# Optimization experiments

Hardware: AMD Instinct MI355X
Metric: run time of the kernel (lower is better)

## Reference

```python
import jax, jax.numpy as jnp
import numpy as np

B, N, H, DH, E, D_IN = 2, 2048, 8, 32, 65536, 256
O = H * DH
SCALE = float(np.sqrt(DH))


def setup_inputs() -> dict:
    key = jax.random.key(0)
    ks = jax.random.split(key, 8)
    rng = np.random.default_rng(0)
    x = jax.random.normal(ks[0], (B, N, D_IN), jnp.float32)
    adj = jax.random.uniform(ks[1], (B, N, N), jnp.float32)
    # unique edges per graph so scatter-add matches torch advanced-index +=
    flat = np.stack([rng.choice(N * N, size=E, replace=False) for _ in range(B)])
    edge_index = jnp.asarray(np.stack([flat // N, flat % N], axis=1), jnp.int32)  # [B,2,E]
    edge_attr = jax.random.normal(ks[2], (B, E, H), jnp.float32)
    mask = jnp.ones((B, N), dtype=bool)
    qkv_w = jax.random.normal(ks[3], (D_IN, 3 * O), jnp.float32) / np.sqrt(D_IN)
    qkv_b = jnp.zeros((3 * O,), jnp.float32)
    e_w1 = jax.random.normal(ks[4], (H, H), jnp.float32) / np.sqrt(H)
    e_b1 = jnp.zeros((H,), jnp.float32)
    e_w2 = jax.random.normal(ks[5], (H, H), jnp.float32) / np.sqrt(H)
    e_b2 = jnp.zeros((H,), jnp.float32)
    shifts = jnp.asarray(np.linspace(0.1, 0.8, H), jnp.float32).reshape(1, H, 1, 1)
    widths = jnp.full((1, H, 1, 1), 0.5, jnp.float32)
    self_loop_W = jnp.asarray(1.0 / DH + rng.uniform(0, 1, H), jnp.float32).reshape(1, H, 1, 1)
    return dict(x=x, adj=adj, edge_attr=edge_attr, qkv_w=qkv_w, qkv_b=qkv_b,
                e_w1=e_w1, e_b1=e_b1, e_w2=e_w2, e_b2=e_b2,
                shifts=shifts, widths=widths, self_loop_W=self_loop_W,
                edge_index=edge_index, mask=mask)


def reference(x, adj, edge_attr, qkv_w, qkv_b, e_w1, e_b1, e_w2, e_b2,
              shifts, widths, self_loop_W, edge_index, mask):
    Bq, Nq = x.shape[0], x.shape[1]
    # qkv projection -> [3,B,H,N,DH]
    qkv = (x @ qkv_w + qkv_b).reshape(Bq, Nq, 3, H, DH)
    qkv = jnp.transpose(qkv, (2, 0, 3, 1, 4))
    Q, K, V = qkv[0], qkv[1], qkv[2]
    # edge FFN applied twice (eval mode: noise/dropout are identity)
    def ffn(e):
        return jax.nn.relu(e @ e_w1 + e_b1) @ e_w2 + e_b2
    ea = ffn(ffn(edge_attr))                      # [B,E,H]
    ea = jnp.transpose(ea, (0, 2, 1))             # [B,H,E]
    # scores + learned moire adjacency bias
    scores = jnp.einsum('bhqd,bhkd->bhqk', Q, K) / SCALE
    moire = jnp.exp(-((adj[:, None] - shifts) ** 2) / (2.0 * widths ** 2))  # gaussian focus
    moire = jnp.clip(moire, 1e-6, None)
    s = scores + jnp.log(moire)                   # [B,H,N,N]
    # scatter edge features into score matrix
    u = edge_index[:, 0, :]                        # [B,E]
    v = edge_index[:, 1, :]
    bi = jnp.arange(Bq)[:, None, None]
    hi = jnp.arange(H)[None, :, None]
    s = s.at[bi, hi, u[:, None, :], v[:, None, :]].add(ea)
    # self-loop diagonal bias (non-trainable)
    s = s + jnp.eye(Nq, dtype=s.dtype)[None, None] * self_loop_W
    # mask and softmax
    m2 = mask[:, None, :] & mask[:, :, None]       # [B,N,N]
    s = jnp.where(m2[:, None], s, jnp.asarray(-1e6, s.dtype))
    attn = jax.nn.softmax(s, axis=-1)
    out = jnp.einsum('bhqk,bhkd->bhqd', attn, V)
    return jnp.transpose(out, (0, 2, 1, 3)).reshape(Bq, Nq, O)
```

## Files before the change

kernel.cpp:

```cpp
#include <hip/hip_runtime.h>

#define B_ 2
#define N_ 2048
#define H_ 8
#define DH_ 32
#define E_ 65536
#define DIN_ 256
#define KT 256
#define NKT (N_ / KT)
#define ECAP 32
#define QSCALE 0.2550348872f
#define LOG2E 1.4426950408889634f
#define LOG2MIN -19.931568569324174f

typedef short bf16x8 __attribute__((ext_vector_type(8)));
typedef float floatx4 __attribute__((ext_vector_type(4)));

__device__ __forceinline__ unsigned short f2b(float f){
  union { float f; unsigned int u; } v; v.f = f;
  return (unsigned short)((v.u + 0x7fffu + ((v.u >> 16) & 1u)) >> 16);
}
__device__ __forceinline__ bf16x8 f8_to_bf(const float* p){
  float4 a = *(const float4*)p, b = *(const float4*)(p + 4);
  bf16x8 r;
// ... 25 lines not shown
    __shared__ float W1[64], W2[64], Bv1[8], Bv2[8];
    if (tid < 64){ W1[tid] = w1[tid]; W2[tid] = w2[tid]; }
    if (tid < 8){ Bv1[tid] = b1[tid]; Bv2[tid] = b2[tid]; }
    __syncthreads();
    int gid = bb * 256 + tid;
    const float* ep = eattr + (size_t)gid * 8;
    float cur[8];
#pragma unroll
    for (int i = 0; i < 8; ++i) cur[i] = ep[i];
#pragma unroll
    for (int pass = 0; pass < 2; ++pass){
      float t[8];
#pragma unroll
      for (int j = 0; j < 8; ++j){
        float s = Bv1[j];
#pragma unroll
        for (int i = 0; i < 8; ++i) s += cur[i] * W1[i * 8 + j];
        t[j] = fmaxf(s, 0.f);
      }
#pragma unroll
      for (int j = 0; j < 8; ++j){
        float s = Bv2[j];
#pragma unroll
        for (int i = 0; i < 8; ++i) s += t[i] * W2[i * 8 + j];
        cur[j] = s;
      }
    }
    float* op = ea + (size_t)gid * 8;
#pragma unroll
    for (int j = 0; j < 8; ++j) op[j] = cur[j] * LOG2E;
  } else if (bb < 1024){
    int gid = (bb - 512) * 256 + tid;
    int b = gid >> 16, e = gid & (E_ - 1);
    int u = ei[(size_t)b * 2 * E_ + e];
    int v = ei[(size_t)b * 2 * E_ + E_ + e];
    int bucket = ((b << 11) + u) * 8 + (v >> 8);
    int slot = atomicAdd(&cnt[bucket], 1);
    if (slot < ECAP) pck[(size_t)bucket * ECAP + slot] = ((unsigned int)e << 11) | (unsigned int)v;
  } else {
    int k = bb - 1024;
    for (int c = tid; c < 768; c += 256)
      wT[(size_t)c * 256 + k] = f2b(w[(size_t)k * 768 + c]);
  }
}

__global__ __launch_bounds__(256) void qkv_kernel(
    const float* __restrict__ x, const unsigned short* __restrict__ wT,
    const float* __restrict__ bias,
    unsigned short* __restrict__ Qb, unsigned short* __restrict__ Kb, unsigned short* __restrict__ Vt)
{
  int tid = threadIdx.x;
  int wave = tid >> 6, lane = tid & 63, m = lane & 15, quad = lane >> 4;
  int rowbase = blockIdx.x * 16;
  int colbase = blockIdx.y * 64 + wave * 16;
  floatx4 acc = {0.f, 0.f, 0.f, 0.f};
#pragma unroll
  for (int kb = 0; kb < 8; ++kb){
    bf16x8 af = f8_to_bf(x + (size_t)(rowbase + m) * DIN_ + kb * 32 + quad * 8);
    bf16x8 bf = *(const bf16x8*)(wT + (size_t)(colbase + m) * DIN_ + kb * 32 + quad * 8);
    acc = __builtin_amdgcn_mfma_f32_16x16x32_bf16(af, bf, acc, 0, 0, 0);
  }
  int ccol = colbase + m;
  int which = ccol >> 8, hh = (ccol >> 5) & 7, dh = ccol & 31;
  float bv = bias[ccol];
  int row0 = rowbase + quad * 4;
  int bidx = row0 >> 11, n0 = row0 & (N_ - 1);
  size_t bh = (size_t)(bidx * H_ + hh);
  if (which == 0){
#pragma unroll
    for (int r = 0; r < 4; ++r)
      Qb[(bh * N_ + n0 + r) * DH_ + dh] = f2b((acc[r] + bv) * QSCALE);
  } else if (which == 1){
#pragma unroll
    for (int r = 0; r < 4; ++r)
      Kb[(bh * N_ + n0 + r) * DH_ + dh] = f2b(acc[r] + bv);
  } else {
    ushort4 st;
    st.x = f2b(acc[0] + bv); st.y = f2b(acc[1] + bv);
    st.z = f2b(acc[2] + bv); st.w = f2b(acc[3] + bv);
    *(ushort4*)(Vt + (bh * DH_ + dh) * N_ + n0) = st;
  }
}

__global__ __launch_bounds__(256) void attn_kernel(
    const unsigned short* __restrict__ Qb, const unsigned short* __restrict__ Kb,
    const unsigned short* __restrict__ Vt, const float* __restrict__ adj,
    const float* __restrict__ ea, const int* __restrict__ cnt, const unsigned int* __restrict__ pck,
    const float* __restrict__ shifts, const float* __restrict__ widths,
    const float* __restrict__ selfW, float* __restrict__ out)
{
  __shared__ float S[4][16][68];
  __shared__ float mfin[4][16], lfin[4][16];

  int bid = blockIdx.x;
  int qt = bid & 127, h = (bid >> 7) & 7, b = bid >> 10;
  int qbase = qt * 16;
  int tid = threadIdx.x, wave = tid >> 6, lane = tid & 63, m = lane & 15, quad = lane >> 4;
  float shift_h = shifts[h];
  float w_h = widths[h];
  float i2w_h = LOG2E / (2.f * w_h * w_h);
  float selfW_h = selfW[h] * LOG2E;
  size_t krow = (size_t)(b * H_ + h) * N_;
  size_t vrow = (size_t)(b * H_ + h) * DH_;
  bf16x8 qfrag = *(const bf16x8*)(Qb + (krow + qbase + m) * DH_ + quad * 8);
  float (*Sw)[68] = S[wave];
  int wcol = wave * 64;

  int rr = lane >> 2, sl0 = lane & 3;
  const int* cntp = cnt + ((size_t)(b * N_) + qbase + rr) * 8;
  const unsigned int* pckp = pck + ((size_t)((b * N_ + qbase + rr) * 8)) * ECAP;
  const float* eabase = ea + (size_t)b * E_ * H_ + h;
  const float* adjp = adj + ((size_t)b * N_ + qbase + m) * N_ + wcol + quad * 8;
  const unsigned short* vp0 = Vt + (vrow + m) * N_ + wcol + quad * 8;
  const unsigned short* vp1 = Vt + (vrow + 16 + m) * N_ + wcol + quad * 8;
  const unsigned short* kp  = Kb + (krow + wcol + m) * DH_ + quad * 8;

  floatx4 sh4 = {shift_h, shift_h, shift_h, shift_h};
  floatx4 ni4 = {-i2w_h, -i2w_h, -i2w_h, -i2w_h};
  floatx4 lm4 = {LOG2MIN, LOG2MIN, LOG2MIN, LOG2MIN};

  float mcur = -1e30f, lcur = 0.f;
  floatx4 oacc0 = {0.f, 0.f, 0.f, 0.f};
  floatx4 oacc1 = {0.f, 0.f, 0.f, 0.f};

  int nb_c = cntp[0]; nb_c = nb_c > ECAP ? ECAP : nb_c;
  unsigned int pk0 = pckp[sl0];
  unsigned int pk1 = pckp[sl0 + 4];
  int c0_c = (int)(pk0 & (N_ - 1)) - wcol;
  int c1_c = (int)(pk1 & (N_ - 1)) - wcol;
  bool g0_c = (sl0 < nb_c) && ((unsigned)c0_c < 64u);
  bool g1_c = (sl0 + 4 < nb_c) && ((unsigned)c1_c < 64u);
  float ea0_c = 0.f, ea1_c = 0.f;
  if (g0_c) ea0_c = eabase[(size_t)(pk0 >> 11) * H_];
  if (g1_c) ea1_c = eabase[(size_t)(pk1 >> 11) * H_];

#pragma unroll
  for (int kt = 0; kt < NKT; ++kt){
    int k0 = kt * KT;
    int nb_n = 0; unsigned int pk0_n = 0, pk1_n = 0;
    if (kt + 1 < NKT){
      nb_n  = cntp[kt + 1];
      pk0_n = pckp[(kt + 1) * ECAP + sl0];
      pk1_n = pckp[(kt + 1) * ECAP + sl0 + 4];
    }
    const float* ap = adjp + k0;
    floatx4 a00 = *(const floatx4*)(ap);
    floatx4 a01 = *(const floatx4*)(ap + 4);
    floatx4 a10 = *(const floatx4*)(ap + 32);
    floatx4 a11 = *(const floatx4*)(ap + 36);

#pragma unroll
    for (int s = 0; s < 4; ++s){
      bf16x8 kf = *(const bf16x8*)(kp + (size_t)(k0 + s * 16) * DH_);
      floatx4 acc = {0.f, 0.f, 0.f, 0.f};
      acc = __builtin_amdgcn_mfma_f32_16x16x32_bf16(qfrag, kf, acc, 0, 0, 0);
#pragma unroll
      for (int r = 0; r < 4; ++r)
        Sw[quad * 4 + r][s * 16 + m] = acc[r];
    }
    {
      int dw = qbase - k0 - wcol;
      if ((unsigned)dw < 64u && lane < 16)
        Sw[lane][dw + lane] += selfW_h;
    }
    if (g0_c) Sw[rr][c0_c] += ea0_c;
    if (g1_c) Sw[rr][c1_c] += ea1_c;
    if (nb_c > 8){
      for (int slot = sl0 + 8; slot < nb_c; slot += 4){
        unsigned int p = pckp[kt * ECAP + slot];
        int vv = (int)(p & (N_ - 1));
        int c = vv - k0 - wcol;
        if ((unsigned)c < 64u) Sw[rr][c] += eabase[(size_t)(p >> 11) * H_];
      }
    }
    int c0_n = 0, c1_n = 0; bool g0_n = false, g1_n = false;
    float ea0_n = 0.f, ea1_n = 0.f;
    if (kt + 1 < NKT){
      nb_n = nb_n > ECAP ? ECAP : nb_n;
      c0_n = (int)(pk0_n & (N_ - 1)) - (k0 + KT) - wcol;
      c1_n = (int)(pk1_n & (N_ - 1)) - (k0 + KT) - wcol;
      g0_n = (sl0 < nb_n) && ((unsigned)c0_n < 64u);
      g1_n = (sl0 + 4 < nb_n) && ((unsigned)c1_n < 64u);
      if (g0_n) ea0_n = eabase[(size_t)(pk0_n >> 11) * H_];
      if (g1_n) ea1_n = eabase[(size_t)(pk1_n >> 11) * H_];
    }
    bf16x8 vf00 = *(const bf16x8*)(vp0 + k0);
    bf16x8 vf01 = *(const bf16x8*)(vp1 + k0);
    bf16x8 vf10 = *(const bf16x8*)(vp0 + k0 + 32);
    bf16x8 vf11 = *(const bf16x8*)(vp1 + k0 + 32);

    const float* sp = &Sw[m][quad * 8];
    floatx4 s00 = *(const floatx4*)(sp);
    floatx4 s01 = *(const floatx4*)(sp + 4);
    floatx4 s10 = *(const floatx4*)(sp + 32);
    floatx4 s11 = *(const floatx4*)(sp + 36);
    floatx4 d;
    d = a00 - sh4; s00 += __builtin_elementwise_max(d * d * ni4, lm4);
    d = a01 - sh4; s01 += __builtin_elementwise_max(d * d * ni4, lm4);
    d = a10 - sh4; s10 += __builtin_elementwise_max(d * d * ni4, lm4);
    d = a11 - sh4; s11 += __builtin_elementwise_max(d * d * ni4, lm4);
    float lm = fmaxf(fmaxf(fmaxf(s00.x, s00.y), fmaxf(s00.z, s00.w)),
                     fmaxf(fmaxf(s01.x, s01.y), fmaxf(s01.z, s01.w)));
    lm = fmaxf(lm, fmaxf(fmaxf(fmaxf(s10.x, s10.y), fmaxf(s10.z, s10.w)),
                         fmaxf(fmaxf(s11.x, s11.y), fmaxf(s11.z, s11.w))));
    lm = fmaxf(lm, __shfl_xor(lm, 16));
    lm = fmaxf(lm, __shfl_xor(lm, 32));
    float mnew = fmaxf(mcur, lm);
    float al = fexp2(mcur - mnew);
    mcur = mnew;
    float al0 = __shfl(al, quad * 4 + 0);
    float al1 = __shfl(al, quad * 4 + 1);
    float al2 = __shfl(al, quad * 4 + 2);
    float al3 = __shfl(al, quad * 4 + 3);
    oacc0[0] *= al0; oacc0[1] *= al1; oacc0[2] *= al2; oacc0[3] *= al3;
    oacc1[0] *= al0; oacc1[1] *= al1; oacc1[2] *= al2; oacc1[3] *= al3;
    floatx4 m4 = {mcur, mcur, mcur, mcur};
    floatx4 e0v = s00 - m4, e1v = s01 - m4, e2v = s10 - m4, e3v = s11 - m4;
    float ps = 0.f, p0, p1;
    union { bf16x8 v; unsigned int u[4]; } P;
    p0 = fexp2(e0v.x); p1 = fexp2(e0v.y); ps += p0 + p1; P.u[0] = cvt_pk_bf16(p0, p1);
    p0 = fexp2(e0v.z); p1 = fexp2(e0v.w); ps += p0 + p1; P.u[1] = cvt_pk_bf16(p0, p1);
    p0 = fexp2(e1v.x); p1 = fexp2(e1v.y); ps += p0 + p1; P.u[2] = cvt_pk_bf16(p0, p1);
    p0 = fexp2(e1v.z); p1 = fexp2(e1v.w); ps += p0 + p1; P.u[3] = cvt_pk_bf16(p0, p1);
    oacc0 = __builtin_amdgcn_mfma_f32_16x16x32_bf16(P.v, vf00, oacc0, 0, 0, 0);
    oacc1 = __builtin_amdgcn_mfma_f32_16x16x32_bf16(P.v, vf01, oacc1, 0, 0, 0);
    p0 = fexp2(e2v.x); p1 = fexp2(e2v.y); ps += p0 + p1; P.u[0] = cvt_pk_bf16(p0, p1);
    p0 = fexp2(e2v.z); p1 = fexp2(e2v.w); ps += p0 + p1; P.u[1] = cvt_pk_bf16(p0, p1);
    p0 = fexp2(e3v.x); p1 = fexp2(e3v.y); ps += p0 + p1; P.u[2] = cvt_pk_bf16(p0, p1);
    p0 = fexp2(e3v.z); p1 = fexp2(e3v.w); ps += p0 + p1; P.u[3] = cvt_pk_bf16(p0, p1);
    oacc0 = __builtin_amdgcn_mfma_f32_16x16x32_bf16(P.v, vf10, oacc0, 0, 0, 0);
    oacc1 = __builtin_amdgcn_mfma_f32_16x16x32_bf16(P.v, vf11, oacc1, 0, 0, 0);
    ps += __shfl_xor(ps, 16);
    ps += __shfl_xor(ps, 32);
    lcur = lcur * al + ps;
    nb_c = nb_n; g0_c = g0_n; g1_c = g1_n;
    c0_c = c0_n; c1_c = c1_n; ea0_c = ea0_n; ea1_c = ea1_n;
  }

  if (quad == 0){ mfin[wave][m] = mcur; lfin[wave][m] = lcur; }
  float* Ow = &S[wave][0][0];
#pragma unroll
  for (int r = 0; r < 4; ++r){
    Ow[(quad * 4 + r) * 32 + m]      = oacc0[r];
    Ow[(quad * 4 + r) * 32 + 16 + m] = oacc1[r];
  }
  __syncthreads();
  const float* Sv = &S[0][0][0];
#pragma unroll
  for (int ii = 0; ii < 2; ++ii){
    int i = tid + ii * 256;
    int r = i >> 5, dcol = i & 31;
    float m0 = mfin[0][r], m1 = mfin[1][r], m2 = mfin[2][r], m3 = mfin[3][r];
    float mg = fmaxf(fmaxf(m0, m1), fmaxf(m2, m3));
    float w0 = fexp2(m0 - mg), w1 = fexp2(m1 - mg);
    float w2 = fexp2(m2 - mg), w3 = fexp2(m3 - mg);
    int o_idx = r * 32 + dcol;
    float o = Sv[o_idx] * w0 + Sv[1088 + o_idx] * w1
            + Sv[2176 + o_idx] * w2 + Sv[3264 + o_idx] * w3;
    float l = lfin[0][r] * w0 + lfin[1][r] * w1 + lfin[2][r] * w2 + lfin[3][r] * w3;
    out[((size_t)b * N_ + qbase + r) * (H_ * DH_) + h * DH_ + dcol] = o / l;
  }
}

extern "C" void kernel_launch(void* const* d_in, const int* in_sizes, int n_in,
                              void* d_out, int out_size, void* d_ws, size_t ws_size,
                              hipStream_t stream)
{
  const float* x      = (const float*)d_in[0];
  const float* adj    = (const float*)d_in[1];
  const float* eattr  = (const float*)d_in[2];
  const float* qkvw   = (const float*)d_in[3];
  const float* qkvb   = (const float*)d_in[4];
  const float* ew1    = (const float*)d_in[5];
  const float* eb1    = (const float*)d_in[6];
  const float* ew2    = (const float*)d_in[7];
  const float* eb2    = (const float*)d_in[8];
  const float* shifts = (const float*)d_in[9];
  const float* widths = (const float*)d_in[10];
  const float* selfW  = (const float*)d_in[11];
  const int*   ei     = (const int*)d_in[12];
  float* out = (float*)d_out;

  char* ws = (char*)d_ws;
  unsigned short* Qb  = (unsigned short*)(ws);
  unsigned short* Kb  = (unsigned short*)(ws + ((size_t)2 << 20));
  unsigned short* Vt  = (unsigned short*)(ws + ((size_t)4 << 20));
  unsigned short* wT  = (unsigned short*)(ws + ((size_t)6 << 20));
  float*          ea  = (float*)(ws + ((size_t)7 << 20));
  int*            cnt = (int*)(ws + ((size_t)11 << 20));
  unsigned int*  pck  = (unsigned int*)(ws + ((size_t)12 << 20));

  hipMemsetAsync(cnt, 0, (size_t)B_ * N_ * 8 * sizeof(int), stream);
  hipLaunchKernelGGL(prep_kernel, dim3(1280), dim3(256), 0, stream,
                     eattr, ew1, eb1, ew2, eb2, ea, ei, cnt, pck, qkvw, wT);
  hipLaunchKernelGGL(qkv_kernel, dim3(256, 12), dim3(256), 0, stream, x, wT, qkvb, Qb, Kb, Vt);
  hipLaunchKernelGGL(attn_kernel, dim3(B_ * H_ * (N_ / 16)), dim3(256), 0, stream,
                     Qb, Kb, Vt, adj, ea, cnt, pck, shifts, widths, selfW, out);
}
```

Before: 235.0 us.

## Keep QK scores in registers via transposed MFMA; stage only sparse deltas in LDS

Computes K·Qᵀ with swapped MFMA operands so each lane holds score columns directly in registers in the layout the P·V MFMA needs. This removes the per-tile round trip of the full score tile through shared memory. Sparse edge and self-loop biases now go into a small per-wave delta buffer in LDS, which is read, zeroed and refilled one tile ahead. In exchange, adj and V are loaded as narrower strided ushort4/float4 pieces, and B fragments are assembled by hand in registers.

```diff
diff --git a/kernel.cpp b/kernel.cpp
--- a/kernel.cpp
+++ b/kernel.cpp
@@ -138,7 +138,7 @@
     const float* __restrict__ shifts, const float* __restrict__ widths,
     const float* __restrict__ selfW, float* __restrict__ out)
 {
-  __shared__ float S[4][16][68];
+  __shared__ float Dlt[4][16][68];
   __shared__ float mfin[4][16], lfin[4][16];
 
   int bid = blockIdx.x;
@@ -152,17 +152,40 @@
   size_t krow = (size_t)(b * H_ + h) * N_;
   size_t vrow = (size_t)(b * H_ + h) * DH_;
   bf16x8 qfrag = *(const bf16x8*)(Qb + (krow + qbase + m) * DH_ + quad * 8);
-  float (*Sw)[68] = S[wave];
+  float (*Dw)[68] = Dlt[wave];
   int wcol = wave * 64;
+
+  floatx4 z4 = {0.f, 0.f, 0.f, 0.f};
+  float* dp0 = &Dw[m][quad * 4];
+  *(floatx4*)(dp0)      = z4;
+  *(floatx4*)(dp0 + 16) = z4;
+  *(floatx4*)(dp0 + 32) = z4;
+  *(floatx4*)(dp0 + 48) = z4;
 
   int rr = lane >> 2, sl0 = lane & 3;
   const int* cntp = cnt + ((size_t)(b * N_) + qbase + rr) * 8;
   const unsigned int* pckp = pck + ((size_t)((b * N_ + qbase + rr) * 8)) * ECAP;
   const float* eabase = ea + (size_t)b * E_ * H_ + h;
-  const float* adjp = adj + ((size_t)b * N_ + qbase + m) * N_ + wcol + quad * 8;
-  const unsigned short* vp0 = Vt + (vrow + m) * N_ + wcol + quad * 8;
-  const unsigned short* vp1 = Vt + (vrow + 16 + m) * N_ + wcol + quad * 8;
+  const float* adjp = adj + ((size_t)b * N_ + qbase + m) * N_ + wcol + quad * 4;
+  const unsigned short* vpA = Vt + (vrow + m) * N_ + wcol + quad * 4;
+  const unsigned short* vpB = Vt + (vrow + 16 + m) * N_ + wcol + quad * 4;
   const unsigned short* kp  = Kb + (krow + wcol + m) * DH_ + quad * 8;
+
+  int ktd = qbase >> 8;
+
+  {
+    int nb0 = cntp[0]; nb0 = nb0 > ECAP ? ECAP : nb0;
+    for (int slot = sl0; slot < nb0; slot += 4){
+      unsigned int p = pckp[slot];
+      int c = (int)(p & (N_ - 1)) - wcol;
+      if ((unsigned)c < 64u)
+        Dw[rr][c] += eabase[(size_t)(p >> 11) * H_];
+    }
+    if (ktd == 0 && lane < 16){
+      int cd = qbase + lane - wcol;
+      if ((unsigned)cd < 64u) Dw[lane][cd] += selfW_h;
+    }
+  }
 
   floatx4 sh4 = {shift_h, shift_h, shift_h, shift_h};
   floatx4 ni4 = {-i2w_h, -i2w_h, -i2w_h, -i2w_h};
@@ -172,20 +195,17 @@
   floatx4 oacc0 = {0.f, 0.f, 0.f, 0.f};
   floatx4 oacc1 = {0.f, 0.f, 0.f, 0.f};
 
-  int nb_c = cntp[0]; nb_c = nb_c > ECAP ? ECAP : nb_c;
-  unsigned int pk0 = pckp[sl0];
-  unsigned int pk1 = pckp[sl0 + 4];
-  int c0_c = (int)(pk0 & (N_ - 1)) - wcol;
-  int c1_c = (int)(pk1 & (N_ - 1)) - wcol;
-  bool g0_c = (sl0 < nb_c) && ((unsigned)c0_c < 64u);
-  bool g1_c = (sl0 + 4 < nb_c) && ((unsigned)c1_c < 64u);
-  float ea0_c = 0.f, ea1_c = 0.f;
-  if (g0_c) ea0_c = eabase[(size_t)(pk0 >> 11) * H_];
-  if (g1_c) ea1_c = eabase[(size_t)(pk1 >> 11) * H_];
-
 #pragma unroll
   for (int kt = 0; kt < NKT; ++kt){
     int k0 = kt * KT;
+    floatx4 d0 = *(const floatx4*)(dp0);
+    floatx4 d1 = *(const floatx4*)(dp0 + 16);
+    floatx4 d2 = *(const floatx4*)(dp0 + 32);
+    floatx4 d3 = *(const floatx4*)(dp0 + 48);
+    *(floatx4*)(dp0)      = z4;
+    *(floatx4*)(dp0 + 16) = z4;
+    *(floatx4*)(dp0 + 32) = z4;
+    *(floatx4*)(dp0 + 48) = z4;
     int nb_n = 0; unsigned int pk0_n = 0, pk1_n = 0;
     if (kt + 1 < NKT){
       nb_n  = cntp[kt + 1];
@@ -193,65 +213,43 @@
       pk1_n = pckp[(kt + 1) * ECAP + sl0 + 4];
     }
     const float* ap = adjp + k0;
-    floatx4 a00 = *(const floatx4*)(ap);
-    floatx4 a01 = *(const floatx4*)(ap + 4);
-    floatx4 a10 = *(const floatx4*)(ap + 32);
-    floatx4 a11 = *(const floatx4*)(ap + 36);
-
-#pragma unroll
-    for (int s = 0; s < 4; ++s){
-      bf16x8 kf = *(const bf16x8*)(kp + (size_t)(k0 + s * 16) * DH_);
-      floatx4 acc = {0.f, 0.f, 0.f, 0.f};
-      acc = __builtin_amdgcn_mfma_f32_16x16x32_bf16(qfrag, kf, acc, 0, 0, 0);
-#pragma unroll
-      for (int r = 0; r < 4; ++r)
-        Sw[quad * 4 + r][s * 16 + m] = acc[r];
-    }
-    {
-      int dw = qbase - k0 - wcol;
-      if ((unsigned)dw < 64u && lane < 16)
-        Sw[lane][dw + lane] += selfW_h;
-    }
-    if (g0_c) Sw[rr][c0_c] += ea0_c;
-    if (g1_c) Sw[rr][c1_c] += ea1_c;
-    if (nb_c > 8){
-      for (int slot = sl0 + 8; slot < nb_c; slot += 4){
-        unsigned int p = pckp[kt * ECAP + slot];
-        int vv = (int)(p & (N_ - 1));
-        int c = vv - k0 - wcol;
-        if ((unsigned)c < 64u) Sw[rr][c] += eabase[(size_t)(p >> 11) * H_];
-      }
-    }
+    floatx4 a0 = *(const floatx4*)(ap);
+    floatx4 a1 = *(const floatx4*)(ap + 16);
+    floatx4 a2 = *(const floatx4*)(ap + 32);
+    floatx4 a3 = *(const floatx4*)(ap + 48);
+    bf16x8 kf0 = *(const bf16x8*)(kp + (size_t)(k0)      * DH_);
+    bf16x8 kf1 = *(const bf16x8*)(kp + (size_t)(k0 + 16) * DH_);
+    bf16x8 kf2 = *(const bf16x8*)(kp + (size_t)(k0 + 32) * DH_);
+    bf16x8 kf3 = *(const bf16x8*)(kp + (size_t)(k0 + 48) * DH_);
+    floatx4 s0 = __builtin_amdgcn_mfma_f32_16x16x32_bf16(kf0, qfrag, z4, 0, 0, 0);
+    floatx4 s1 = __builtin_amdgcn_mfma_f32_16x16x32_bf16(kf1, qfrag, z4, 0, 0, 0);
+    floatx4 s2 = __builtin_amdgcn_mfma_f32_16x16x32_bf16(kf2, qfrag, z4, 0, 0, 0);
+    floatx4 s3 = __builtin_amdgcn_mfma_f32_16x16x32_bf16(kf3, qfrag, z4, 0, 0, 0);
+    const unsigned short* vA = vpA + k0;
+    const unsigned short* vB = vpB + k0;
+    ushort4 vA0 = *(const ushort4*)(vA);      ushort4 vA1 = *(const ushort4*)(vA + 16);
+    ushort4 vA2 = *(const ushort4*)(vA + 32); ushort4 vA3 = *(const ushort4*)(vA + 48);
+    ushort4 vB0 = *(const ushort4*)(vB);      ushort4 vB1 = *(const ushort4*)(vB + 16);
+    ushort4 vB2 = *(const ushort4*)(vB + 32); ushort4 vB3 = *(const ushort4*)(vB + 48);
     int c0_n = 0, c1_n = 0; bool g0_n = false, g1_n = false;
     float ea0_n = 0.f, ea1_n = 0.f;
     if (kt + 1 < NKT){
       nb_n = nb_n > ECAP ? ECAP : nb_n;
-      c0_n = (int)(pk0_n & (N_ - 1)) - (k0 + KT) - wcol;
-      c1_n = (int)(pk1_n & (N_ - 1)) - (k0 + KT) - wcol;
-      g0_n = (sl0 < nb_n) && ((unsigned)c0_n < 64u);
-      g1_n = (sl0 + 4 < nb_n) && ((unsigned)c1_n < 64u);
+      c0_n = (int)(pk0_n & (N_ - 1)) - wcol;
+      c1_n = (int)(pk1_n & (N_ - 1)) - wcol;
+      g0_n = (sl0 < nb_n) && ((unsigned)(c0_n - (k0 + KT)) < 64u);
+      g1_n = (sl0 + 4 < nb_n) && ((unsigned)(c1_n - (k0 + KT)) < 64u);
       if (g0_n) ea0_n = eabase[(size_t)(pk0_n >> 11) * H_];
       if (g1_n) ea1_n = eabase[(size_t)(pk1_n >> 11) * H_];
     }
-    bf16x8 vf00 = *(const bf16x8*)(vp0 + k0);
-    bf16x8 vf01 = *(const bf16x8*)(vp1 + k0);
-    bf16x8 vf10 = *(const bf16x8*)(vp0 + k0 + 32);
-    bf16x8 vf11 = *(const bf16x8*)(vp1 + k0 + 32);
-
-    const float* sp = &Sw[m][quad * 8];
-    floatx4 s00 = *(const floatx4*)(sp);
-    floatx4 s01 = *(const floatx4*)(sp + 4);
-    floatx4 s10 = *(const floatx4*)(sp + 32);
-    floatx4 s11 = *(const floatx4*)(sp + 36);
-    floatx4 d;
-    d = a00 - sh4; s00 += __builtin_elementwise_max(d * d * ni4, lm4);
-    d = a01 - sh4; s01 += __builtin_elementwise_max(d * d * ni4, lm4);
-    d = a10 - sh4; s10 += __builtin_elementwise_max(d * d * ni4, lm4);
-    d = a11 - sh4; s11 += __builtin_elementwise_max(d * d * ni4, lm4);
-    float lm = fmaxf(fmaxf(fmaxf(s00.x, s00.y), fmaxf(s00.z, s00.w)),
-                     fmaxf(fmaxf(s01.x, s01.y), fmaxf(s01.z, s01.w)));
-    lm = fmaxf(lm, fmaxf(fmaxf(fmaxf(s10.x, s10.y), fmaxf(s10.z, s10.w)),
-                         fmaxf(fmaxf(s11.x, s11.y), fmaxf(s11.z, s11.w))));
+    floatx4 t;
+    t = a0 - sh4; s0 += d0 + __builtin_elementwise_max(t * t * ni4, lm4);
+    t = a1 - sh4; s1 += d1 + __builtin_elementwise_max(t * t * ni4, lm4);
+    t = a2 - sh4; s2 += d2 + __builtin_elementwise_max(t * t * ni4, lm4);
+    t = a3 - sh4; s3 += d3 + __builtin_elementwise_max(t * t * ni4, lm4);
+    floatx4 mxv = __builtin_elementwise_max(__builtin_elementwise_max(s0, s1),
+                                            __builtin_elementwise_max(s2, s3));
+    float lm = fmaxf(fmaxf(mxv.x, mxv.y), fmaxf(mxv.z, mxv.w));
     lm = fmaxf(lm, __shfl_xor(lm, 16));
     lm = fmaxf(lm, __shfl_xor(lm, 32));
     float mnew = fmaxf(mcur, lm);
@@ -263,38 +261,60 @@
     float al3 = __shfl(al, quad * 4 + 3);
     oacc0[0] *= al0; oacc0[1] *= al1; oacc0[2] *= al2; oacc0[3] *= al3;
     oacc1[0] *= al0; oacc1[1] *= al1; oacc1[2] *= al2; oacc1[3] *= al3;
-    floatx4 m4 = {mcur, mcur, mcur, mcur};
-    floatx4 e0v = s00 - m4, e1v = s01 - m4, e2v = s10 - m4, e3v = s11 - m4;
-    float ps = 0.f, p0, p1;
-    union { bf16x8 v; unsigned int u[4]; } P;
-    p0 = fexp2(e0v.x); p1 = fexp2(e0v.y); ps += p0 + p1; P.u[0] = cvt_pk_bf16(p0, p1);
-    p0 = fexp2(e0v.z); p1 = fexp2(e0v.w); ps += p0 + p1; P.u[1] = cvt_pk_bf16(p0, p1);
-    p0 = fexp2(e1v.x); p1 = fexp2(e1v.y); ps += p0 + p1; P.u[2] = cvt_pk_bf16(p0, p1);
-    p0 = fexp2(e1v.z); p1 = fexp2(e1v.w); ps += p0 + p1; P.u[3] = cvt_pk_bf16(p0, p1);
-    oacc0 = __builtin_amdgcn_mfma_f32_16x16x32_bf16(P.v, vf00, oacc0, 0, 0, 0);
-    oacc1 = __builtin_amdgcn_mfma_f32_16x16x32_bf16(P.v, vf01, oacc1, 0, 0, 0);
-    p0 = fexp2(e2v.x); p1 = fexp2(e2v.y); ps += p0 + p1; P.u[0] = cvt_pk_bf16(p0, p1);
-    p0 = fexp2(e2v.z); p1 = fexp2(e2v.w); ps += p0 + p1; P.u[1] = cvt_pk_bf16(p0, p1);
-    p0 = fexp2(e3v.x); p1 = fexp2(e3v.y); ps += p0 + p1; P.u[2] = cvt_pk_bf16(p0, p1);
-    p0 = fexp2(e3v.z); p1 = fexp2(e3v.w); ps += p0 + p1; P.u[3] = cvt_pk_bf16(p0, p1);
-    oacc0 = __builtin_amdgcn_mfma_f32_16x16x32_bf16(P.v, vf10, oacc0, 0, 0, 0);
-    oacc1 = __builtin_amdgcn_mfma_f32_16x16x32_bf16(P.v, vf11, oacc1, 0, 0, 0);
+    floatx4 mb = {mcur, mcur, mcur, mcur};
+    floatx4 e0 = s0 - mb, e1 = s1 - mb, e2 = s2 - mb, e3 = s3 - mb;
+    floatx4 p0, p1, p2, p3;
+    p0.x = fexp2(e0.x); p0.y = fexp2(e0.y); p0.z = fexp2(e0.z); p0.w = fexp2(e0.w);
+    p1.x = fexp2(e1.x); p1.y = fexp2(e1.y); p1.z = fexp2(e1.z); p1.w = fexp2(e1.w);
+    p2.x = fexp2(e2.x); p2.y = fexp2(e2.y); p2.z = fexp2(e2.z); p2.w = fexp2(e2.w);
+    p3.x = fexp2(e3.x); p3.y = fexp2(e3.y); p3.z = fexp2(e3.z); p3.w = fexp2(e3.w);
+    floatx4 psv = (p0 + p1) + (p2 + p3);
+    float ps = (psv.x + psv.y) + (psv.z + psv.w);
+    union { bf16x8 v; unsigned int u[4]; } A0, A1;
+    A0.u[0] = cvt_pk_bf16(p0.x, p0.y); A0.u[1] = cvt_pk_bf16(p0.z, p0.w);
+    A0.u[2] = cvt_pk_bf16(p1.x, p1.y); A0.u[3] = cvt_pk_bf16(p1.z, p1.w);
+    A1.u[0] = cvt_pk_bf16(p2.x, p2.y); A1.u[1] = cvt_pk_bf16(p2.z, p2.w);
+    A1.u[2] = cvt_pk_bf16(p3.x, p3.y); A1.u[3] = cvt_pk_bf16(p3.z, p3.w);
+    bf16x8 B00, B01, B10, B11;
+    B00[0] = (short)vA0.x; B00[1] = (short)vA0.y; B00[2] = (short)vA0.z; B00[3] = (short)vA0.w;
+    B00[4] = (short)vA1.x; B00[5] = (short)vA1.y; B00[6] = (short)vA1.z; B00[7] = (short)vA1.w;
+    B01[0] = (short)vB0.x; B01[1] = (short)vB0.y; B01[2] = (short)vB0.z; B01[3] = (short)vB0.w;
+    B01[4] = (short)vB1.x; B01[5] = (short)vB1.y; B01[6] = (short)vB1.z; B01[7] = (short)vB1.w;
+    B10[0] = (short)vA2.x; B10[1] = (short)vA2.y; B10[2] = (short)vA2.z; B10[3] = (short)vA2.w;
+    B10[4] = (short)vA3.x; B10[5] = (short)vA3.y; B10[6] = (short)vA3.z; B10[7] = (short)vA3.w;
+    B11[0] = (short)vB2.x; B11[1] = (short)vB2.y; B11[2] = (short)vB2.z; B11[3] = (short)vB2.w;
+    B11[4] = (short)vB3.x; B11[5] = (short)vB3.y; B11[6] = (short)vB3.z; B11[7] = (short)vB3.w;
+    oacc0 = __builtin_amdgcn_mfma_f32_16x16x32_bf16(A0.v, B00, oacc0, 0, 0, 0);
+    oacc1 = __builtin_amdgcn_mfma_f32_16x16x32_bf16(A0.v, B01, oacc1, 0, 0, 0);
+    oacc0 = __builtin_amdgcn_mfma_f32_16x16x32_bf16(A1.v, B10, oacc0, 0, 0, 0);
+    oacc1 = __builtin_amdgcn_mfma_f32_16x16x32_bf16(A1.v, B11, oacc1, 0, 0, 0);
     ps += __shfl_xor(ps, 16);
     ps += __shfl_xor(ps, 32);
     lcur = lcur * al + ps;
-    nb_c = nb_n; g0_c = g0_n; g1_c = g1_n;
-    c0_c = c0_n; c1_c = c1_n; ea0_c = ea0_n; ea1_c = ea1_n;
+    if (g0_n) Dw[rr][c0_n - (k0 + KT)] += ea0_n;
+    if (g1_n) Dw[rr][c1_n - (k0 + KT)] += ea1_n;
+    if (nb_n > 8){
+      for (int slot = sl0 + 8; slot < nb_n; slot += 4){
+        unsigned int p = pckp[(kt + 1) * ECAP + slot];
+        int c = (int)(p & (N_ - 1)) - (k0 + KT) - wcol;
+        if ((unsigned)c < 64u) Dw[rr][c] += eabase[(size_t)(p >> 11) * H_];
+      }
+    }
+    if (kt + 1 == ktd && lane < 16){
+      int cd = qbase + lane - (kt + 1) * KT - wcol;
+      if ((unsigned)cd < 64u) Dw[lane][cd] += selfW_h;
+    }
   }
 
   if (quad == 0){ mfin[wave][m] = mcur; lfin[wave][m] = lcur; }
-  float* Ow = &S[wave][0][0];
+  float* Ow = &Dlt[wave][0][0];
 #pragma unroll
   for (int r = 0; r < 4; ++r){
     Ow[(quad * 4 + r) * 32 + m]      = oacc0[r];
     Ow[(quad * 4 + r) * 32 + 16 + m] = oacc1[r];
   }
   __syncthreads();
-  const float* Sv = &S[0][0][0];
+  const float* Sv = &Dlt[0][0][0];
 #pragma unroll
   for (int ii = 0; ii < 2; ++ii){
     int i = tid + ii * 256;
```

Measured after the change: 260.7 us. 11.0% more time.

## Process two 16-row query tiles per attention block and remap blocks across XCDs

Applied to the files above, without the earlier changes.

Each attention block now handles 32 query rows as two independent 16-row chains that share the K and V fragment loads. This halves the global loads of K and V per query row. Block indices are also remapped so that all heads of the same query region land on the same XCD, which should improve L2 reuse of the adjacency and edge data. In exchange the block uses more registers and twice the shared memory, launches half as many blocks, and adds a launch-bounds occupancy hint.

```diff
diff --git a/kernel.cpp b/kernel.cpp
--- a/kernel.cpp
+++ b/kernel.cpp
@@ -131,19 +131,22 @@
   }
 }
 
-__global__ __launch_bounds__(256) void attn_kernel(
+__global__ __launch_bounds__(256, 4) void attn_kernel(
     const unsigned short* __restrict__ Qb, const unsigned short* __restrict__ Kb,
     const unsigned short* __restrict__ Vt, const float* __restrict__ adj,
     const float* __restrict__ ea, const int* __restrict__ cnt, const unsigned int* __restrict__ pck,
     const float* __restrict__ shifts, const float* __restrict__ widths,
     const float* __restrict__ selfW, float* __restrict__ out)
 {
-  __shared__ float S[4][16][68];
-  __shared__ float mfin[4][16], lfin[4][16];
+  __shared__ float S2[2][4][16][68];
+  __shared__ float mfin[2][4][16], lfin[2][4][16];
 
   int bid = blockIdx.x;
-  int qt = bid & 127, h = (bid >> 7) & 7, b = bid >> 10;
-  int qbase = qt * 16;
+  int xcd = bid & 7, idx = bid >> 3;
+  int h = idx & 7;
+  int bqp = xcd * 16 + (idx >> 3);
+  int b = bqp >> 6, qp = bqp & 63;
+  int qbaseA = qp * 32, qbaseB = qbaseA + 16;
   int tid = threadIdx.x, wave = tid >> 6, lane = tid & 63, m = lane & 15, quad = lane >> 4;
   float shift_h = shifts[h];
   float w_h = widths[h];
@@ -151,15 +154,20 @@
   float selfW_h = selfW[h] * LOG2E;
   size_t krow = (size_t)(b * H_ + h) * N_;
   size_t vrow = (size_t)(b * H_ + h) * DH_;
-  bf16x8 qfrag = *(const bf16x8*)(Qb + (krow + qbase + m) * DH_ + quad * 8);
-  float (*Sw)[68] = S[wave];
+  bf16x8 qfragA = *(const bf16x8*)(Qb + (krow + qbaseA + m) * DH_ + quad * 8);
+  bf16x8 qfragB = *(const bf16x8*)(Qb + (krow + qbaseB + m) * DH_ + quad * 8);
+  float (*SwA)[68] = S2[0][wave];
+  float (*SwB)[68] = S2[1][wave];
   int wcol = wave * 64;
 
   int rr = lane >> 2, sl0 = lane & 3;
-  const int* cntp = cnt + ((size_t)(b * N_) + qbase + rr) * 8;
-  const unsigned int* pckp = pck + ((size_t)((b * N_ + qbase + rr) * 8)) * ECAP;
+  const int* cntpA = cnt + ((size_t)(b * N_) + qbaseA + rr) * 8;
+  const int* cntpB = cntpA + 128;
+  const unsigned int* pckpA = pck + ((size_t)((b * N_ + qbaseA + rr) * 8)) * ECAP;
+  const unsigned int* pckpB = pckpA + 128 * ECAP;
   const float* eabase = ea + (size_t)b * E_ * H_ + h;
-  const float* adjp = adj + ((size_t)b * N_ + qbase + m) * N_ + wcol + quad * 8;
+  const float* adjpA = adj + ((size_t)b * N_ + qbaseA + m) * N_ + wcol + quad * 8;
+  const float* adjpB = adjpA + (size_t)16 * N_;
   const unsigned short* vp0 = Vt + (vrow + m) * N_ + wcol + quad * 8;
   const unsigned short* vp1 = Vt + (vrow + 16 + m) * N_ + wcol + quad * 8;
   const unsigned short* kp  = Kb + (krow + wcol + m) * DH_ + quad * 8;
@@ -167,147 +175,231 @@
   floatx4 sh4 = {shift_h, shift_h, shift_h, shift_h};
   floatx4 ni4 = {-i2w_h, -i2w_h, -i2w_h, -i2w_h};
   floatx4 lm4 = {LOG2MIN, LOG2MIN, LOG2MIN, LOG2MIN};
-
-  float mcur = -1e30f, lcur = 0.f;
-  floatx4 oacc0 = {0.f, 0.f, 0.f, 0.f};
-  floatx4 oacc1 = {0.f, 0.f, 0.f, 0.f};
-
-  int nb_c = cntp[0]; nb_c = nb_c > ECAP ? ECAP : nb_c;
-  unsigned int pk0 = pckp[sl0];
-  unsigned int pk1 = pckp[sl0 + 4];
-  int c0_c = (int)(pk0 & (N_ - 1)) - wcol;
-  int c1_c = (int)(pk1 & (N_ - 1)) - wcol;
-  bool g0_c = (sl0 < nb_c) && ((unsigned)c0_c < 64u);
-  bool g1_c = (sl0 + 4 < nb_c) && ((unsigned)c1_c < 64u);
-  float ea0_c = 0.f, ea1_c = 0.f;
-  if (g0_c) ea0_c = eabase[(size_t)(pk0 >> 11) * H_];
-  if (g1_c) ea1_c = eabase[(size_t)(pk1 >> 11) * H_];
+  floatx4 z4  = {0.f, 0.f, 0.f, 0.f};
+
+  float mcurA = -1e30f, lcurA = 0.f;
+  float mcurB = -1e30f, lcurB = 0.f;
+  floatx4 oA0 = z4, oA1 = z4, oB0 = z4, oB1 = z4;
+
+  int nbA = cntpA[0]; nbA = nbA > ECAP ? ECAP : nbA;
+  int nbB = cntpB[0]; nbB = nbB > ECAP ? ECAP : nbB;
+  unsigned int pA0 = pckpA[sl0], pA1 = pckpA[sl0 + 4];
+  unsigned int pB0 = pckpB[sl0], pB1 = pckpB[sl0 + 4];
+  int cA0 = (int)(pA0 & (N_ - 1)) - wcol, cA1 = (int)(pA1 & (N_ - 1)) - wcol;
+  int cB0 = (int)(pB0 & (N_ - 1)) - wcol, cB1 = (int)(pB1 & (N_ - 1)) - wcol;
+  bool gA0 = (sl0 < nbA) && ((unsigned)cA0 < 64u);
+  bool gA1 = (sl0 + 4 < nbA) && ((unsigned)cA1 < 64u);
+  bool gB0 = (sl0 < nbB) && ((unsigned)cB0 < 64u);
+  bool gB1 = (sl0 + 4 < nbB) && ((unsigned)cB1 < 64u);
+  float eA0 = 0.f, eA1 = 0.f, eB0 = 0.f, eB1 = 0.f;
+  if (gA0) eA0 = eabase[(size_t)(pA0 >> 11) * H_];
+  if (gA1) eA1 = eabase[(size_t)(pA1 >> 11) * H_];
+  if (gB0) eB0 = eabase[(size_t)(pB0 >> 11) * H_];
+  if (gB1) eB1 = eabase[(size_t)(pB1 >> 11) * H_];
 
 #pragma unroll
   for (int kt = 0; kt < NKT; ++kt){
     int k0 = kt * KT;
-    int nb_n = 0; unsigned int pk0_n = 0, pk1_n = 0;
+    int nbA_n = 0, nbB_n = 0;
+    unsigned int pA0_n = 0, pA1_n = 0, pB0_n = 0, pB1_n = 0;
     if (kt + 1 < NKT){
-      nb_n  = cntp[kt + 1];
-      pk0_n = pckp[(kt + 1) * ECAP + sl0];
-      pk1_n = pckp[(kt + 1) * ECAP + sl0 + 4];
-    }
-    const float* ap = adjp + k0;
-    floatx4 a00 = *(const floatx4*)(ap);
-    floatx4 a01 = *(const floatx4*)(ap + 4);
-    floatx4 a10 = *(const floatx4*)(ap + 32);
-    floatx4 a11 = *(const floatx4*)(ap + 36);
+      nbA_n = cntpA[kt + 1];            nbB_n = cntpB[kt + 1];
+      pA0_n = pckpA[(kt + 1) * ECAP + sl0];  pA1_n = pckpA[(kt + 1) * ECAP + sl0 + 4];
+      pB0_n = pckpB[(kt + 1) * ECAP + sl0];  pB1_n = pckpB[(kt + 1) * ECAP + sl0 + 4];
+    }
+    const float* apA = adjpA + k0;
+    const float* apB = adjpB + k0;
+    floatx4 aA00 = *(const floatx4*)(apA);      floatx4 aA01 = *(const floatx4*)(apA + 4);
+    floatx4 aA10 = *(const floatx4*)(apA + 32); floatx4 aA11 = *(const floatx4*)(apA + 36);
+    floatx4 aB00 = *(const floatx4*)(apB);      floatx4 aB01 = *(const floatx4*)(apB + 4);
+    floatx4 aB10 = *(const floatx4*)(apB + 32); floatx4 aB11 = *(const floatx4*)(apB + 36);
 
 #pragma unroll
     for (int s = 0; s < 4; ++s){
       bf16x8 kf = *(const bf16x8*)(kp + (size_t)(k0 + s * 16) * DH_);
-      floatx4 acc = {0.f, 0.f, 0.f, 0.f};
-      acc = __builtin_amdgcn_mfma_f32_16x16x32_bf16(qfrag, kf, acc, 0, 0, 0);
-#pragma unroll
-      for (int r = 0; r < 4; ++r)
-        Sw[quad * 4 + r][s * 16 + m] = acc[r];
+      floatx4 accA = __builtin_amdgcn_mfma_f32_16x16x32_bf16(qfragA, kf, z4, 0, 0, 0);
+      floatx4 accB = __builtin_amdgcn_mfma_f32_16x16x32_bf16(qfragB, kf, z4, 0, 0, 0);
+#pragma unroll
+      for (int r = 0; r < 4; ++r){
+        SwA[quad * 4 + r][s * 16 + m] = accA[r];
+        SwB[quad * 4 + r][s * 16 + m] = accB[r];
+      }
     }
     {
-      int dw = qbase - k0 - wcol;
-      if ((unsigned)dw < 64u && lane < 16)
-        Sw[lane][dw + lane] += selfW_h;
-    }
-    if (g0_c) Sw[rr][c0_c] += ea0_c;
-    if (g1_c) Sw[rr][c1_c] += ea1_c;
-    if (nb_c > 8){
-      for (int slot = sl0 + 8; slot < nb_c; slot += 4){
-        unsigned int p = pckp[kt * ECAP + slot];
-        int vv = (int)(p & (N_ - 1));
-        int c = vv - k0 - wcol;
-        if ((unsigned)c < 64u) Sw[rr][c] += eabase[(size_t)(p >> 11) * H_];
+      int dwA = qbaseA - k0 - wcol;
+      if ((unsigned)dwA < 64u && lane < 16) SwA[lane][dwA + lane] += selfW_h;
+      int dwB = qbaseB - k0 - wcol;
+      if ((unsigned)dwB < 64u && lane < 16) SwB[lane][dwB + lane] += selfW_h;
+    }
+    if (gA0) SwA[rr][cA0] += eA0;
+    if (gA1) SwA[rr][cA1] += eA1;
+    if (gB0) SwB[rr][cB0] += eB0;
+    if (gB1) SwB[rr][cB1] += eB1;
+    if (nbA > 8){
+      for (int slot = sl0 + 8; slot < nbA; slot += 4){
+        unsigned int p = pckpA[kt * ECAP + slot];
+        int c = (int)(p & (N_ - 1)) - k0 - wcol;
+        if ((unsigned)c < 64u) SwA[rr][c] += eabase[(size_t)(p >> 11) * H_];
       }
     }
-    int c0_n = 0, c1_n = 0; bool g0_n = false, g1_n = false;
-    float ea0_n = 0.f, ea1_n = 0.f;
+    if (nbB > 8){
+      for (int slot = sl0 + 8; slot < nbB; slot += 4){
+        unsigned int p = pckpB[kt * ECAP + slot];
+        int c = (int)(p & (N_ - 1)) - k0 - wcol;
+        if ((unsigned)c < 64u) SwB[rr][c] += eabase[(size_t)(p >> 11) * H_];
+      }
+    }
+    int cA0_n = 0, cA1_n = 0, cB0_n = 0, cB1_n = 0;
+    bool gA0_n = false, gA1_n = false, gB0_n = false, gB1_n = false;
+    float eA0_n = 0.f, eA1_n = 0.f, eB0_n = 0.f, eB1_n = 0.f;
     if (kt + 1 < NKT){
-      nb_n = nb_n > ECAP ? ECAP : nb_n;
-      c0_n = (int)(pk0_n & (N_ - 1)) - (k0 + KT) - wcol;
-      c1_n = (int)(pk1_n & (N_ - 1)) - (k0 + KT) - wcol;
-      g0_n = (sl0 < nb_n) && ((unsigned)c0_n < 64u);
-      g1_n = (sl0 + 4 < nb_n) && ((unsigned)c1_n < 64u);
-      if (g0_n) ea0_n = eabase[(size_t)(pk0_n >> 11) * H_];
-      if (g1_n) ea1_n = eabase[(size_t)(pk1_n >> 11) * H_];
+      nbA_n = nbA_n > ECAP ? ECAP : nbA_n;
+      nbB_n = nbB_n > ECAP ? ECAP : nbB_n;
+      cA0_n = (int)(pA0_n & (N_ - 1)) - (k0 + KT) - wcol;
+      cA1_n = (int)(pA1_n & (N_ - 1)) - (k0 + KT) - wcol;
+      cB0_n = (int)(pB0_n & (N_ - 1)) - (k0 + KT) - wcol;
+      cB1_n = (int)(pB1_n & (N_ - 1)) - (k0 + KT) - wcol;
+      gA0_n = (sl0 < nbA_n) && ((unsigned)cA0_n < 64u);
+      gA1_n = (sl0 + 4 < nbA_n) && ((unsigned)cA1_n < 64u);
+      gB0_n = (sl0 < nbB_n) && ((unsigned)cB0_n < 64u);
+      gB1_n = (sl0 + 4 < nbB_n) && ((unsigned)cB1_n < 64u);
+      if (gA0_n) eA0_n = eabase[(size_t)(pA0_n >> 11) * H_];
+      if (gA1_n) eA1_n = eabase[(size_t)(pA1_n >> 11) * H_];
+      if (gB0_n) eB0_n = eabase[(size_t)(pB0_n >> 11) * H_];
+      if (gB1_n) eB1_n = eabase[(size_t)(pB1_n >> 11) * H_];
     }
     bf16x8 vf00 = *(const bf16x8*)(vp0 + k0);
     bf16x8 vf01 = *(const bf16x8*)(vp1 + k0);
     bf16x8 vf10 = *(const bf16x8*)(vp0 + k0 + 32);
     bf16x8 vf11 = *(const bf16x8*)(vp1 + k0 + 32);
 
-    const float* sp = &Sw[m][quad * 8];
-    floatx4 s00 = *(const floatx4*)(sp);
-    floatx4 s01 = *(const floatx4*)(sp + 4);
-    floatx4 s10 = *(const floatx4*)(sp + 32);
-    floatx4 s11 = *(const floatx4*)(sp + 36);
-    floatx4 d;
-    d = a00 - sh4; s00 += __builtin_elementwise_max(d * d * ni4, lm4);
-    d = a01 - sh4; s01 += __builtin_elementwise_max(d * d * ni4, lm4);
-    d = a10 - sh4; s10 += __builtin_elementwise_max(d * d * ni4, lm4);
-    d = a11 - sh4; s11 += __builtin_elementwise_max(d * d * ni4, lm4);
-    float lm = fmaxf(fmaxf(fmaxf(s00.x, s00.y), fmaxf(s00.z, s00.w)),
-                     fmaxf(fmaxf(s01.x, s01.y), fmaxf(s01.z, s01.w)));
-    lm = fmaxf(lm, fmaxf(fmaxf(fmaxf(s10.x, s10.y), fmaxf(s10.z, s10.w)),
-                         fmaxf(fmaxf(s11.x, s11.y), fmaxf(s11.z, s11.w))));
-    lm = fmaxf(lm, __shfl_xor(lm, 16));
-    lm = fmaxf(lm, __shfl_xor(lm, 32));
-    float mnew = fmaxf(mcur, lm);
-    float al = fexp2(mcur - mnew);
-    mcur = mnew;
-    float al0 = __shfl(al, quad * 4 + 0);
-    float al1 = __shfl(al, quad * 4 + 1);
-    float al2 = __shfl(al, quad * 4 + 2);
-    float al3 = __shfl(al, quad * 4 + 3);
-    oacc0[0] *= al0; oacc0[1] *= al1; oacc0[2] *= al2; oacc0[3] *= al3;
-    oacc1[0] *= al0; oacc1[1] *= al1; oacc1[2] *= al2; oacc1[3] *= al3;
-    floatx4 m4 = {mcur, mcur, mcur, mcur};
-    floatx4 e0v = s00 - m4, e1v = s01 - m4, e2v = s10 - m4, e3v = s11 - m4;
-    float ps = 0.f, p0, p1;
-    union { bf16x8 v; unsigned int u[4]; } P;
-    p0 = fexp2(e0v.x); p1 = fexp2(e0v.y); ps += p0 + p1; P.u[0] = cvt_pk_bf16(p0, p1);
-    p0 = fexp2(e0v.z); p1 = fexp2(e0v.w); ps += p0 + p1; P.u[1] = cvt_pk_bf16(p0, p1);
-    p0 = fexp2(e1v.x); p1 = fexp2(e1v.y); ps += p0 + p1; P.u[2] = cvt_pk_bf16(p0, p1);
-    p0 = fexp2(e1v.z); p1 = fexp2(e1v.w); ps += p0 + p1; P.u[3] = cvt_pk_bf16(p0, p1);
-    oacc0 = __builtin_amdgcn_mfma_f32_16x16x32_bf16(P.v, vf00, oacc0, 0, 0, 0);
-    oacc1 = __builtin_amdgcn_mfma_f32_16x16x32_bf16(P.v, vf01, oacc1, 0, 0, 0);
-    p0 = fexp2(e2v.x); p1 = fexp2(e2v.y); ps += p0 + p1; P.u[0] = cvt_pk_bf16(p0, p1);
-    p0 = fexp2(e2v.z); p1 = fexp2(e2v.w); ps += p0 + p1; P.u[1] = cvt_pk_bf16(p0, p1);
-    p0 = fexp2(e3v.x); p1 = fexp2(e3v.y); ps += p0 + p1; P.u[2] = cvt_pk_bf16(p0, p1);
-    p0 = fexp2(e3v.z); p1 = fexp2(e3v.w); ps += p0 + p1; P.u[3] = cvt_pk_bf16(p0, p1);
-    oacc0 = __builtin_amdgcn_mfma_f32_16x16x32_bf16(P.v, vf10, oacc0, 0, 0, 0);
-    oacc1 = __builtin_amdgcn_mfma_f32_16x16x32_bf16(P.v, vf11, oacc1, 0, 0, 0);
-    ps += __shfl_xor(ps, 16);
-    ps += __shfl_xor(ps, 32);
-    lcur = lcur * al + ps;
-    nb_c = nb_n; g0_c = g0_n; g1_c = g1_n;
-    c0_c = c0_n; c1_c = c1_n; ea0_c = ea0_n; ea1_c = ea1_n;
-  }
-
-  if (quad == 0){ mfin[wave][m] = mcur; lfin[wave][m] = lcur; }
-  float* Ow = &S[wave][0][0];
+    {
+      const float* sp = &SwA[m][quad * 8];
+      floatx4 s00 = *(const floatx4*)(sp);
+      floatx4 s01 = *(const floatx4*)(sp + 4);
+      floatx4 s10 = *(const floatx4*)(sp + 32);
+      floatx4 s11 = *(const floatx4*)(sp + 36);
+      floatx4 d;
+      d = aA00 - sh4; s00 += __builtin_elementwise_max(d * d * ni4, lm4);
+      d = aA01 - sh4; s01 += __builtin_elementwise_max(d * d * ni4, lm4);
+      d = aA10 - sh4; s10 += __builtin_elementwise_max(d * d * ni4, lm4);
+      d = aA11 - sh4; s11 += __builtin_elementwise_max(d * d * ni4, lm4);
+      float lm = fmaxf(fmaxf(fmaxf(s00.x, s00.y), fmaxf(s00.z, s00.w)),
+                       fmaxf(fmaxf(s01.x, s01.y), fmaxf(s01.z, s01.w)));
+      lm = fmaxf(lm, fmaxf(fmaxf(fmaxf(s10.x, s10.y), fmaxf(s10.z, s10.w)),
+                           fmaxf(fmaxf(s11.x, s11.y), fmaxf(s11.z, s11.w))));
+      lm = fmaxf(lm, __shfl_xor(lm, 16));
+      lm = fmaxf(lm, __shfl_xor(lm, 32));
+      float mnew = fmaxf(mcurA, lm);
+      float al = fexp2(mcurA - mnew);
+      mcurA = mnew;
+      float al0 = __shfl(al, quad * 4 + 0);
+      float al1 = __shfl(al, quad * 4 + 1);
+      float al2 = __shfl(al, quad * 4 + 2);
+      float al3 = __shfl(al, quad * 4 + 3);
+      oA0[0] *= al0; oA0[1] *= al1; oA0[2] *= al2; oA0[3] *= al3;
+      oA1[0] *= al0; oA1[1] *= al1; oA1[2] *= al2; oA1[3] *= al3;
+      floatx4 m4 = {mcurA, mcurA, mcurA, mcurA};
+      floatx4 e0v = s00 - m4, e1v = s01 - m4, e2v = s10 - m4, e3v = s11 - m4;
+      float ps = 0.f, p0, p1;
+      union { bf16x8 v; unsigned int u[4]; } P;
+      p0 = fexp2(e0v.x); p1 = fexp2(e0v.y); ps += p0 + p1; P.u[0] = cvt_pk_bf16(p0, p1);
+      p0 = fexp2(e0v.z); p1 = fexp2(e0v.w); ps += p0 + p1; P.u[1] = cvt_pk_bf16(p0, p1);
+      p0 = fexp2(e1v.x); p1 = fexp2(e1v.y); ps += p0 + p1; P.u[2] = cvt_pk_bf16(p0, p1);
+      p0 = fexp2(e1v.z); p1 = fexp2(e1v.w); ps += p0 + p1; P.u[3] = cvt_pk_bf16(p0, p1);
+      oA0 = __builtin_amdgcn_mfma_f32_16x16x32_bf16(P.v, vf00, oA0, 0, 0, 0);
+      oA1 = __builtin_amdgcn_mfma_f32_16x16x32_bf16(P.v, vf01, oA1, 0, 0, 0);
+      p0 = fexp2(e2v.x); p1 = fexp2(e2v.y); ps += p0 + p1; P.u[0] = cvt_pk_bf16(p0, p1);
+      p0 = fexp2(e2v.z); p1 = fexp2(e2v.w); ps += p0 + p1; P.u[1] = cvt_pk_bf16(p0, p1);
+      p0 = fexp2(e3v.x); p1 = fexp2(e3v.y); ps += p0 + p1; P.u[2] = cvt_pk_bf16(p0, p1);
+      p0 = fexp2(e3v.z); p1 = fexp2(e3v.w); ps += p0 + p1; P.u[3] = cvt_pk_bf16(p0, p1);
+      oA0 = __builtin_amdgcn_mfma_f32_16x16x32_bf16(P.v, vf10, oA0, 0, 0, 0);
+      oA1 = __builtin_amdgcn_mfma_f32_16x16x32_bf16(P.v, vf11, oA1, 0, 0, 0);
+      ps += __shfl_xor(ps, 16);
+      ps += __shfl_xor(ps, 32);
+      lcurA = lcurA * al + ps;
+    }
+    {
+      const float* sp = &SwB[m][quad * 8];
+      floatx4 s00 = *(const floatx4*)(sp);
+      floatx4 s01 = *(const floatx4*)(sp + 4);
+      floatx4 s10 = *(const floatx4*)(sp + 32);
+      floatx4 s11 = *(const floatx4*)(sp + 36);
+      floatx4 d;
+      d = aB00 - sh4; s00 += __builtin_elementwise_max(d * d * ni4, lm4);
+      d = aB01 - sh4; s01 += __builtin_elementwise_max(d * d * ni4, lm4);
+      d = aB10 - sh4; s10 += __builtin_elementwise_max(d * d * ni4, lm4);
+      d = aB11 - sh4; s11 += __builtin_elementwise_max(d * d * ni4, lm4);
+      float lm = fmaxf(fmaxf(fmaxf(s00.x, s00.y), fmaxf(s00.z, s00.w)),
+                       fmaxf(fmaxf(s01.x, s01.y), fmaxf(s01.z, s01.w)));
+      lm = fmaxf(lm, fmaxf(fmaxf(fmaxf(s10.x, s10.y), fmaxf(s10.z, s10.w)),
+                           fmaxf(fmaxf(s11.x, s11.y), fmaxf(s11.z, s11.w))));
+      lm = fmaxf(lm, __shfl_xor(lm, 16));
+      lm = fmaxf(lm, __shfl_xor(lm, 32));
+      float mnew = fmaxf(mcurB, lm);
+      float al = fexp2(mcurB - mnew);
+      mcurB = mnew;
+      float al0 = __shfl(al, quad * 4 + 0);
+      float al1 = __shfl(al, quad * 4 + 1);
+      float al2 = __shfl(al, quad * 4 + 2);
+      float al3 = __shfl(al, quad * 4 + 3);
+      oB0[0] *= al0; oB0[1] *= al1; oB0[2] *= al2; oB0[3] *= al3;
+      oB1[0] *= al0; oB1[1] *= al1; oB1[2] *= al2; oB1[3] *= al3;
+      floatx4 m4 = {mcurB, mcurB, mcurB, mcurB};
+      floatx4 e0v = s00 - m4, e1v = s01 - m4, e2v = s10 - m4, e3v = s11 - m4;
+      float ps = 0.f, p0, p1;
+      union { bf16x8 v; unsigned int u[4]; } P;
+      p0 = fexp2(e0v.x); p1 = fexp2(e0v.y); ps += p0 + p1; P.u[0] = cvt_pk_bf16(p0, p1);
+      p0 = fexp2(e0v.z); p1 = fexp2(e0v.w); ps += p0 + p1; P.u[1] = cvt_pk_bf16(p0, p1);
+      p0 = fexp2(e1v.x); p1 = fexp2(e1v.y); ps += p0 + p1; P.u[2] = cvt_pk_bf16(p0, p1);
+      p0 = fexp2(e1v.z); p1 = fexp2(e1v.w); ps += p0 + p1; P.u[3] = cvt_pk_bf16(p0, p1);
+      oB0 = __builtin_amdgcn_mfma_f32_16x16x32_bf16(P.v, vf00, oB0, 0, 0, 0);
+      oB1 = __builtin_amdgcn_mfma_f32_16x16x32_bf16(P.v, vf01, oB1, 0, 0, 0);
+      p0 = fexp2(e2v.x); p1 = fexp2(e2v.y); ps += p0 + p1; P.u[0] = cvt_pk_bf16(p0, p1);
+      p0 = fexp2(e2v.z); p1 = fexp2(e2v.w); ps += p0 + p1; P.u[1] = cvt_pk_bf16(p0, p1);
+      p0 = fexp2(e3v.x); p1 = fexp2(e3v.y); ps += p0 + p1; P.u[2] = cvt_pk_bf16(p0, p1);
+      p0 = fexp2(e3v.z); p1 = fexp2(e3v.w); ps += p0 + p1; P.u[3] = cvt_pk_bf16(p0, p1);
+      oB0 = __builtin_amdgcn_mfma_f32_16x16x32_bf16(P.v, vf10, oB0, 0, 0, 0);
+      oB1 = __builtin_amdgcn_mfma_f32_16x16x32_bf16(P.v, vf11, oB1, 0, 0, 0);
+      ps += __shfl_xor(ps, 16);
+      ps += __shfl_xor(ps, 32);
+      lcurB = lcurB * al + ps;
+    }
+    nbA = nbA_n; gA0 = gA0_n; gA1 = gA1_n; cA0 = cA0_n; cA1 = cA1_n; eA0 = eA0_n; eA1 = eA1_n;
+    nbB = nbB_n; gB0 = gB0_n; gB1 = gB1_n; cB0 = cB0_n; cB1 = cB1_n; eB0 = eB0_n; eB1 = eB1_n;
+  }
+
+  if (quad == 0){
+    mfin[0][wave][m] = mcurA; lfin[0][wave][m] = lcurA;
+    mfin[1][wave][m] = mcurB; lfin[1][wave][m] = lcurB;
+  }
+  float* OwA = &S2[0][wave][0][0];
+  float* OwB = &S2[1][wave][0][0];
 #pragma unroll
   for (int r = 0; r < 4; ++r){
-    Ow[(quad * 4 + r) * 32 + m]      = oacc0[r];
-    Ow[(quad * 4 + r) * 32 + 16 + m] = oacc1[r];
+    OwA[(quad * 4 + r) * 32 + m]      = oA0[r];
+    OwA[(quad * 4 + r) * 32 + 16 + m] = oA1[r];
+    OwB[(quad * 4 + r) * 32 + m]      = oB0[r];
+    OwB[(quad * 4 + r) * 32 + 16 + m] = oB1[r];
   }
   __syncthreads();
-  const float* Sv = &S[0][0][0];
-#pragma unroll
-  for (int ii = 0; ii < 2; ++ii){
+#pragma unroll
+  for (int ii = 0; ii < 4; ++ii){
     int i = tid + ii * 256;
-    int r = i >> 5, dcol = i & 31;
-    float m0 = mfin[0][r], m1 = mfin[1][r], m2 = mfin[2][r], m3 = mfin[3][r];
+    int chain = i >> 9, r = (i >> 5) & 15, dcol = i & 31;
+    const float* Sv = &S2[chain][0][0][0];
+    float m0 = mfin[chain][0][r], m1 = mfin[chain][1][r];
+    float m2 = mfin[chain][2][r], m3 = mfin[chain][3][r];
     float mg = fmaxf(fmaxf(m0, m1), fmaxf(m2, m3));
     float w0 = fexp2(m0 - mg), w1 = fexp2(m1 - mg);
     float w2 = fexp2(m2 - mg), w3 = fexp2(m3 - mg);
     int o_idx = r * 32 + dcol;
     float o = Sv[o_idx] * w0 + Sv[1088 + o_idx] * w1
             + Sv[2176 + o_idx] * w2 + Sv[3264 + o_idx] * w3;
-    float l = lfin[0][r] * w0 + lfin[1][r] * w1 + lfin[2][r] * w2 + lfin[3][r] * w3;
-    out[((size_t)b * N_ + qbase + r) * (H_ * DH_) + h * DH_ + dcol] = o / l;
+    float l = lfin[chain][0][r] * w0 + lfin[chain][1][r] * w1
+            + lfin[chain][2][r] * w2 + lfin[chain][3][r] * w3;
+    int qb = chain ? qbaseB : qbaseA;
+    out[((size_t)b * N_ + qb + r) * (H_ * DH_) + h * DH_ + dcol] = o / l;
   }
 }
 
@@ -343,6 +435,6 @@
   hipLaunchKernelGGL(prep_kernel, dim3(1280), dim3(256), 0, stream,
                      eattr, ew1, eb1, ew2, eb2, ea, ei, cnt, pck, qkvw, wT);
   hipLaunchKernelGGL(qkv_kernel, dim3(256, 12), dim3(256), 0, stream, x, wT, qkvb, Qb, Kb, Vt);
-  hipLaunchKernelGGL(attn_kernel, dim3(B_ * H_ * (N_ / 16)), dim3(256), 0, stream,
+  hipLaunchKernelGGL(attn_kernel, dim3(B_ * H_ * (N_ / 32)), dim3(256), 0, stream,
                      Qb, Kb, Vt, adj, ea, cnt, pck, shifts, widths, selfW, out);
 }
```

New measurement: 239.3 us. No clear change (+1.8%).
